# Kernel optimization log

Measured on AMD Instinct MI355X. Metric: run time of the kernel, lower is better.

## Reference

```python
import jax, jax.numpy as jnp
import numpy as np

VOCAB, EMB, HID, NCLS = 50257, 48, 128, 2000
B, S = 512, 1024


def setup_inputs() -> dict:
    key = jax.random.key(0)
    ks = jax.random.split(key, 8)
    x = jax.random.randint(ks[0], (B, S), 0, VOCAB)
    emb_table = jax.random.normal(ks[1], (VOCAB, EMB), dtype=jnp.float32)
    emb_table = emb_table.at[0].set(0.0)  # padding_idx=0
    k_ih = 1.0 / np.sqrt(HID)
    w_ih = jax.random.uniform(ks[2], (4 * HID, EMB), minval=-k_ih, maxval=k_ih, dtype=jnp.float32)
    w_hh = jax.random.uniform(ks[3], (4 * HID, HID), minval=-k_ih, maxval=k_ih, dtype=jnp.float32)
    b_ih = jax.random.uniform(ks[4], (4 * HID,), minval=-k_ih, maxval=k_ih, dtype=jnp.float32)
    b_hh = jax.random.uniform(ks[5], (4 * HID,), minval=-k_ih, maxval=k_ih, dtype=jnp.float32)
    k_fc = 1.0 / np.sqrt(HID)
    w_fc = jax.random.uniform(ks[6], (NCLS, HID), minval=-k_fc, maxval=k_fc, dtype=jnp.float32)
    b_fc = jax.random.uniform(ks[7], (NCLS,), minval=-k_fc, maxval=k_fc, dtype=jnp.float32)
    return {"x": x, "emb_table": emb_table, "w_ih": w_ih, "w_hh": w_hh,
            "b_ih": b_ih, "b_hh": b_hh, "w_fc": w_fc, "b_fc": b_fc}


def _lstm_last_hidden(e, w_ih, w_hh, b_ih, b_hh):
    # e: [B, S, E]. Precompute input contributions for all timesteps (one big GEMM).
    xg = jnp.einsum('bse,ge->bsg', e, w_ih) + b_ih + b_hh  # [B, S, 4H]
    xg = jnp.transpose(xg, (1, 0, 2))                      # [S, B, 4H]
    Bn = e.shape[0]
    h0 = jnp.zeros((Bn, HID), e.dtype)
    c0 = jnp.zeros((Bn, HID), e.dtype)

    def step(carry, xg_t):
        h, c = carry
        g = xg_t + h @ w_hh.T                              # [B, 4H]
        i, f, gg, o = jnp.split(g, 4, axis=-1)             # PyTorch gate order i,f,g,o
        i = jax.nn.sigmoid(i)
        f = jax.nn.sigmoid(f)
        gg = jnp.tanh(gg)
        o = jax.nn.sigmoid(o)
        c = f * c + i * gg
        h = o * jnp.tanh(c)
        return (h, c), None

    (h_n, _), _ = jax.lax.scan(step, (h0, c0), xg)
    return h_n


def reference(x, emb_table, w_ih, w_hh, b_ih, b_hh, w_fc, b_fc):
    e = emb_table[x]                                       # [B, S, E] gather
    h_n = _lstm_last_hidden(e, w_ih, w_hh, b_ih, b_hh)     # [B, H]
    return h_n @ w_fc.T + b_fc                             # [B, NCLS]
```

## Files before the change

### kernel.cpp

```cpp
#include <hip/hip_runtime.h>

#define DI __device__ __forceinline__

typedef unsigned int uint;
typedef unsigned short ushort;
typedef _Float16 half2t __attribute__((ext_vector_type(2)));
typedef _Float16 f16x8 __attribute__((ext_vector_type(8)));
typedef float f32x4 __attribute__((ext_vector_type(4)));

#define VOCAB 50257
#define NEMB 48
#define HID 128
#define G4 512
#define NCLS 2000
#define BATCH 512
#define SEQ 1024

DI float sigm(float x) {
  return __builtin_amdgcn_rcpf(1.0f + __builtin_amdgcn_exp2f(-1.4426950408889634f * x));
}
DI float tanhfast(float x) {
  return 1.0f - 2.0f * __builtin_amdgcn_rcpf(__builtin_amdgcn_exp2f(2.8853900817779268f * x) + 1.0f);
}

DI void barrier_lds_only() {
  asm volatile("s_waitcnt lgkmcnt(0)" ::: "memory");
  __builtin_amdgcn_s_barrier();
  asm volatile("" ::: "memory");
}

#define VROWS 32
__global__ __launch_bounds__(512) void build_P(
    const float* __restrict__ emb, const float* __restrict__ w_ih,
    const float* __restrict__ b_ih, const float* __restrict__ b_hh,
    _Float16* __restrict__ P)
{
  __shared__ __align__(16) float eL[VROWS][NEMB];
  const int tid = threadIdx.x;
  const int v0 = blockIdx.x * VROWS;
  int nrows = VOCAB - v0; if (nrows > VROWS) nrows = VROWS;

  for (int f = tid; f < nrows * NEMB; f += 512)
    eL[f / NEMB][f % NEMB] = emb[(size_t)v0 * NEMB + f];

  float w[NEMB];
  {
    const float* wr = w_ih + (size_t)tid * NEMB;
#pragma unroll
    for (int k = 0; k < NEMB; k++) w[k] = wr[k];
  }
  float bias = b_ih[tid] + b_hh[tid];
  const int pidx = ((tid & 127) << 2) + (tid >> 7);
  __syncthreads();

  for (int v = 0; v < nrows; v++) {
    const float4* e4 = (const float4*)&eL[v][0];
    float a = bias;
#pragma unroll
    for (int k = 0; k < NEMB / 4; k++) {
      float4 e = e4[k];
      a += w[4 * k] * e.x + w[4 * k + 1] * e.y + w[4 * k + 2] * e.z + w[4 * k + 3] * e.w;
    }
    P[(size_t)(v0 + v) * G4 + pidx] = (_Float16)a;
  }
}

__global__ __launch_bounds__(512, 4) void lstm_mfma5(
    const int* __restrict__ x, const float* __restrict__ w_hh,
    const _Float16* __restrict__ P, float* __restrict__ hout)
{
  __shared__ ushort tokL[SEQ];
  __shared__ __align__(16) _Float16 hbuf[2][16][HID];

  const int tid  = threadIdx.x;
  const int lane = tid & 63;
  const int wave = tid >> 6;
  const int l15  = lane & 15;
  const int lg   = lane >> 4;
  const int u    = wave * 16 + l15;
  const int blk  = blockIdx.x;

  {
    const int* xp = x + (size_t)blk * SEQ;
#pragma unroll
    for (int i = 0; i < SEQ / 512; i++) tokL[tid + 512 * i] = (ushort)xp[tid + 512 * i];
  }
  {
    uint4 z; z.x = z.y = z.z = z.w = 0u;
    ((uint4*)hbuf)[tid] = z;
  }

  f16x8 Bf[4][4];
#pragma unroll
  for (int g = 0; g < 4; g++) {
    const float* wr = w_hh + (size_t)(g * 128 + u) * HID + lg * 8;
#pragma unroll
    for (int ck = 0; ck < 4; ck++) {
      const float4* p4 = (const float4*)(wr + ck * 32);
      float4 wa = p4[0], wb = p4[1];
      f16x8 f;
      f[0] = (_Float16)wa.x; f[1] = (_Float16)wa.y;
      f[2] = (_Float16)wa.z; f[3] = (_Float16)wa.w;
      f[4] = (_Float16)wb.x; f[5] = (_Float16)wb.y;
      f[6] = (_Float16)wb.z; f[7] = (_Float16)wb.w;
      Bf[g][ck] = f;
    }
  }

  int aoff[4];
#pragma unroll
  for (int ck = 0; ck < 4; ck++)
    aoff[ck] = l15 * 256 + ((((ck * 4 + lg) ^ l15)) << 4);

  const int hwoff0 = u * 2;
  float cst0 = 0.0f;

  __syncthreads();

  uint2 xgA0 = {0, 0}, xgB0 = {0, 0};
  if (lg == 0) {
    xgA0 = *(const uint2*)(P + (size_t)tokL[0] * G4 + u * 4);
    xgB0 = *(const uint2*)(P + (size_t)tokL[1] * G4 + u * 4);
  }

  const f32x4 fz = {0.f, 0.f, 0.f, 0.f};
  const char* hB = (const char*)hbuf;
  char* hW = (char*)hbuf;

#define MF(Areg, ckk, a0, a1, a2, a3) do {                                     \
    a0 = __builtin_amdgcn_mfma_f32_16x16x32_f16(Areg, Bf[0][ckk], a0, 0, 0, 0);\
    a1 = __builtin_amdgcn_mfma_f32_16x16x32_f16(Areg, Bf[1][ckk], a1, 0, 0, 0);\
    a2 = __builtin_amdgcn_mfma_f32_16x16x32_f16(Areg, Bf[2][ckk], a2, 0, 0, 0);\
    a3 = __builtin_amdgcn_mfma_f32_16x16x32_f16(Areg, Bf[3][ckk], a3, 0, 0, 0);\
  } while (0)

#define STEP(t, par) do {                                                      \
    const char* hc = hB + (par) * 4096;                                        \
    f16x8 A0 = *(const f16x8*)(hc + aoff[0]);                                  \
    f16x8 A1 = *(const f16x8*)(hc + aoff[1]);                                  \
    f16x8 A2 = *(const f16x8*)(hc + aoff[2]);                                  \
    f16x8 A3 = *(const f16x8*)(hc + aoff[3]);                                  \
    f32x4 a0 = fz, a1 = fz, a2 = fz, a3 = fz;                                  \
    MF(A0, 0, a0, a1, a2, a3);                                                 \
    MF(A1, 1, a0, a1, a2, a3);                                                 \
    MF(A2, 2, a0, a1, a2, a3);                                                 \
    MF(A3, 3, a0, a1, a2, a3);                                                 \
    if (lg == 0) {                                                             \
      uint2 xc0 = (par) ? xgB0 : xgA0;           \
      int tc = (t) + 2; if (tc > SEQ - 1) tc = SEQ - 1;                        \
      int tk0 = tokL[tc];                                                      \
      uint2 v0 = *(const uint2*)(P + (size_t)tk0 * G4 + u * 4);                \
      if (par) xgB0 = v0; else xgA0 = v0;                                      \
      char* hn = hW + ((par) ^ 1) * 4096;                                      \
      half2t x0 = __builtin_bit_cast(half2t, xc0.x);                           \
      half2t x1 = __builtin_bit_cast(half2t, xc0.y);                           \
      float gi = a0[0] + (float)x0.x;                                          \
      float gf = a1[0] + (float)x0.y;                                          \
      float gc = a2[0] + (float)x1.x;                                          \
      float go = a3[0] + (float)x1.y;                                          \
      float fi = sigm(gi), ff = sigm(gf), gt = tanhfast(gc), fo = sigm(go);    \
      cst0 = ff * cst0 + fi * gt;                                              \
      float hh = fo * tanhfast(cst0);                                          \
      *(_Float16*)(hn + hwoff0) = (_Float16)hh;                                \
      if ((t) == SEQ - 1)                                                      \
        hout[(size_t)blk * HID + u] = hh;                                      \
    }                                                                          \
    barrier_lds_only();                                                        \
  } while (0)

  for (int t = 0; t < SEQ; t += 2) { STEP(t, 0); STEP(t + 1, 1); }
#undef STEP
#undef MF
}

typedef _Float16 h2 __attribute__((ext_vector_type(2)));
DI float fdot2f(h2 a, h2 b, float c) { return c + (float)a.x * (float)b.x + (float)a.y * (float)b.y; }

__global__ __launch_bounds__(512, 4) void lstm_scan_fb(
    const int* __restrict__ x, const float* __restrict__ emb,
    const float* __restrict__ w_ih, const float* __restrict__ w_hh,
    const float* __restrict__ b_ih, const float* __restrict__ b_hh,
    float* __restrict__ hout)
{
  __shared__ int tokL[SEQ];
  __shared__ __align__(16) _Float16 h16[HID];
  __shared__ float g2h[2][G4];
  __shared__ __align__(8) h2 e16[2][NEMB / 2];

  const int tid = threadIdx.x;
  const int b = blockIdx.x;
  const int col = tid & 255;
  const int kh = tid >> 8;
  const int koff = kh * (HID / 2);

  {
    const int* xp = x + (size_t)b * SEQ;
#pragma unroll
    for (int i = 0; i < SEQ / 512; i++) tokL[tid + 512 * i] = xp[tid + 512 * i];
  }

  h2 w0[HID / 4], w1[HID / 4];
  {
    const float4* wr0 = (const float4*)(w_hh + (size_t)col * HID + koff);
    const float4* wr1 = (const float4*)(w_hh + (size_t)(col + 256) * HID + koff);
#pragma unroll
    for (int k = 0; k < HID / 8; k++) {
      float4 a = wr0[k];
      h2 p; p.x = (_Float16)a.x; p.y = (_Float16)a.y; w0[2 * k] = p;
      p.x = (_Float16)a.z; p.y = (_Float16)a.w; w0[2 * k + 1] = p;
      float4 bv = wr1[k];
      p.x = (_Float16)bv.x; p.y = (_Float16)bv.y; w1[2 * k] = p;
      p.x = (_Float16)bv.z; p.y = (_Float16)bv.w; w1[2 * k + 1] = p;
    }
  }
  h2 wih0[NEMB / 2], wih1[NEMB / 2];
  float bias0 = 0.0f, bias1 = 0.0f;
  if (kh == 0) {
    const float* wr0 = w_ih + (size_t)col * NEMB;
    const float* wr1 = w_ih + (size_t)(col + 256) * NEMB;
#pragma unroll
    for (int k = 0; k < NEMB / 2; k++) {
      h2 p;
      p.x = (_Float16)wr0[2 * k]; p.y = (_Float16)wr0[2 * k + 1]; wih0[k] = p;
      p.x = (_Float16)wr1[2 * k]; p.y = (_Float16)wr1[2 * k + 1]; wih1[k] = p;
    }
    bias0 = b_ih[col] + b_hh[col];
    bias1 = b_ih[col + 256] + b_hh[col + 256];
  }
  if (tid < HID) h16[tid] = (_Float16)0.0f;
  __syncthreads();

  float c = 0.0f;
  float2 einfl = {0.0f, 0.0f};
  if (tid < NEMB / 2) {
    float2 e0 = ((const float2*)(emb + (size_t)tokL[0] * NEMB))[tid];
    einfl    = ((const float2*)(emb + (size_t)tokL[1] * NEMB))[tid];
    h2 p; p.x = (_Float16)e0.x; p.y = (_Float16)e0.y;
    e16[0][tid] = p;
  }
  __syncthreads();

#define STEPF(t, par) do {                                                     \
    float xg0, xg1;                                                            \
    if (tid < NEMB / 2) {                                                      \
      int tc = (t) + 2; if (tc > SEQ - 1) tc = SEQ - 1;                        \
      h2 p; p.x = (_Float16)einfl.x; p.y = (_Float16)einfl.y;                  \
      e16[((t) + 1) & 1][tid] = p;                                             \
      einfl = ((const float2*)(emb + (size_t)tokL[tc] * NEMB))[tid];           \
    }                                                                          \
    if (kh == 0) {                                                             \
      xg0 = bias0; xg1 = bias1;                                                \
      _Pragma("unroll")                                                        \
      for (int k = 0; k < NEMB / 2; k++) {                                     \
        xg0 = fdot2f(wih0[k], e16[(par)][k], xg0);                             \
        xg1 = fdot2f(wih1[k], e16[(par)][k], xg1);                             \
      }                                                                        \
    } else { xg0 = 0.0f; xg1 = 0.0f; }                                         \
    const uint4* hv = (const uint4*)h16 + (kh << 3);                           \
    float s0 = xg0, u0 = 0.0f, s1 = xg1, u1 = 0.0f;                            \
    _Pragma("unroll")                                                          \
    for (int kt = 0; kt < HID / 16; kt++) {                                    \
      uint4 hq = hv[kt];                                                       \
      h2 ha = __builtin_bit_cast(h2, hq.x);                                    \
      h2 hb = __builtin_bit_cast(h2, hq.y);                                    \
      h2 hc = __builtin_bit_cast(h2, hq.z);                                    \
      h2 hd = __builtin_bit_cast(h2, hq.w);                                    \
      s0 = fdot2f(w0[4 * kt + 0], ha, s0);                                     \
      u0 = fdot2f(w0[4 * kt + 1], hb, u0);                                     \
      s0 = fdot2f(w0[4 * kt + 2], hc, s0);                                     \
      u0 = fdot2f(w0[4 * kt + 3], hd, u0);                                     \
      s1 = fdot2f(w1[4 * kt + 0], ha, s1);                                     \
      u1 = fdot2f(w1[4 * kt + 1], hb, u1);                                     \
      s1 = fdot2f(w1[4 * kt + 2], hc, s1);                                     \
      u1 = fdot2f(w1[4 * kt + 3], hd, u1);                                     \
    }                                                                          \
    g2h[kh][col] = s0 + u0;                                                    \
    g2h[kh][col + 256] = s1 + u1;                                              \
    barrier_lds_only();                                                        \
    if (tid < HID) {                                                           \
      float gi = g2h[0][tid]           + g2h[1][tid];                          \
      float gf = g2h[0][HID + tid]     + g2h[1][HID + tid];                    \
      float gc = g2h[0][2 * HID + tid] + g2h[1][2 * HID + tid];                \
      float go = g2h[0][3 * HID + tid] + g2h[1][3 * HID + tid];                \
      float fi = sigm(gi), ff = sigm(gf), gt = tanhfast(gc), fo = sigm(go);    \
      c = ff * c + fi * gt;                                                    \
      float hh = fo * tanhfast(c);                                             \
      h16[tid] = (_Float16)hh;                                                 \
      if ((t) == SEQ - 1) hout[(size_t)b * HID + tid] = hh;                    \
    }                                                                          \
    barrier_lds_only();                                                        \
  } while (0)

  for (int t = 0; t < SEQ; t += 2) { STEPF(t, 0); STEPF(t + 1, 1); }
#undef STEPF
}

#define FCR 64
#define FCC 64
__global__ __launch_bounds__(256) void fc_kernel(
    const float* __restrict__ h, const float* __restrict__ w_fc,
    const float* __restrict__ b_fc, float* __restrict__ out)
{
  __shared__ float aT[HID][FCR];
  __shared__ float bT[HID][FCC];
  const int tid = threadIdx.x;
  const int r0 = blockIdx.y * FCR;
  const int c0 = blockIdx.x * FCC;

  for (int f = tid; f < FCR * (HID / 4); f += 256) {
    int row = f >> 5, q = f & 31;
    float4 v = ((const float4*)h)[(((size_t)(r0 + row)) << 5) + q];
    aT[4 * q + 0][row] = v.x; aT[4 * q + 1][row] = v.y;
    aT[4 * q + 2][row] = v.z; aT[4 * q + 3][row] = v.w;
    int wrow = c0 + row;
    float4 wv;
    if (wrow < NCLS) wv = ((const float4*)w_fc)[(((size_t)wrow) << 5) + q];
    else { wv.x = 0.f; wv.y = 0.f; wv.z = 0.f; wv.w = 0.f; }
    bT[4 * q + 0][row] = wv.x; bT[4 * q + 1][row] = wv.y;
    bT[4 * q + 2][row] = wv.z; bT[4 * q + 3][row] = wv.w;
  }
  __syncthreads();

  const int cr = tid & 15, rr = tid >> 4;
  float acc[4][4];
#pragma unroll
  for (int i = 0; i < 4; i++)
#pragma unroll
    for (int j = 0; j < 4; j++) acc[i][j] = 0.0f;

#pragma unroll 4
  for (int k = 0; k < HID; k++) {
    float4 av = *(const float4*)&aT[k][4 * rr];
    float4 bv = *(const float4*)&bT[k][4 * cr];
    float a[4] = {av.x, av.y, av.z, av.w};
    float bb[4] = {bv.x, bv.y, bv.z, bv.w};
#pragma unroll
    for (int i = 0; i < 4; i++)
#pragma unroll
      for (int j = 0; j < 4; j++) acc[i][j] += a[i] * bb[j];
  }

#pragma unroll
  for (int j = 0; j < 4; j++) {
    int cc = c0 + 4 * cr + j;
    if (cc < NCLS) {
      float bias = b_fc[cc];
#pragma unroll
      for (int i = 0; i < 4; i++)
        out[(size_t)(r0 + 4 * rr + i) * NCLS + cc] = acc[i][j] + bias;
    }
  }
}

extern "C" void kernel_launch(void* const* d_in, const int* in_sizes, int n_in,
                              void* d_out, int out_size, void* d_ws, size_t ws_size,
                              hipStream_t stream) {
  const int*   xx   = (const int*)d_in[0];
  const float* emb  = (const float*)d_in[1];
  const float* w_ih = (const float*)d_in[2];
  const float* w_hh = (const float*)d_in[3];
  const float* b_ih = (const float*)d_in[4];
  const float* b_hh = (const float*)d_in[5];
  const float* w_fc = (const float*)d_in[6];
  const float* b_fc = (const float*)d_in[7];
  float* out = (float*)d_out;

  const size_t pbytes = (size_t)VOCAB * G4 * sizeof(_Float16);
  const size_t palign = (pbytes + 255) & ~(size_t)255;
  const size_t hbytes = (size_t)BATCH * HID * sizeof(float);

  float* hout;
  if (ws_size >= palign + hbytes) {
    _Float16* P = (_Float16*)d_ws;
    hout = (float*)((char*)d_ws + palign);
    build_P<<<(VOCAB + VROWS - 1) / VROWS, 512, 0, stream>>>(emb, w_ih, b_ih, b_hh, P);
    lstm_mfma5<<<BATCH, 512, 0, stream>>>(xx, w_hh, P, hout);
  } else {
    hout = (float*)d_ws;
    lstm_scan_fb<<<BATCH, 512, 0, stream>>>(xx, emb, w_ih, w_hh, b_ih, b_hh, hout);
  }
  dim3 fcg((NCLS + FCC - 1) / FCC, BATCH / FCR);
  fc_kernel<<<fcg, 256, 0, stream>>>(hout, w_fc, b_fc, out);
}
```

Measured before the change: 965.4 us.

## Process two batch rows per LSTM block using spare MFMA rows

Each LSTM block now advances two sequences at once, halving the grid to 256 blocks. The second sequence occupies row 1 of the 16-row MFMA A tile, which was previously zero-padded, so the recurrent matmul per step costs about the same. Row-1 gate results are passed through a small LDS exchange buffer to lanes 16-31, which compute that sequence's cell update. The h write offset uses a swizzle that matches the A-load addressing. The intent is to get more useful work out of each latency-bound step, at the cost of an extra LDS round trip inside the step and fewer resident waves per CU.

```diff
diff --git a/kernel.cpp b/kernel.cpp
--- a/kernel.cpp
+++ b/kernel.cpp
@@ -15,6 +15,8 @@
 #define NCLS 2000
 #define BATCH 512
 #define SEQ 1024
+#define MROWS 2
+#define NBLK2 (BATCH / MROWS)
 
 DI float sigm(float x) {
   return __builtin_amdgcn_rcpf(1.0f + __builtin_amdgcn_exp2f(-1.4426950408889634f * x));
@@ -65,12 +67,13 @@
   }
 }
 
-__global__ __launch_bounds__(512, 4) void lstm_mfma5(
+__global__ __launch_bounds__(512, 2) void lstm_mfma6(
     const int* __restrict__ x, const float* __restrict__ w_hh,
     const _Float16* __restrict__ P, float* __restrict__ hout)
 {
-  __shared__ ushort tokL[SEQ];
+  __shared__ ushort tokL[MROWS][SEQ];
   __shared__ __align__(16) _Float16 hbuf[2][16][HID];
+  __shared__ float xch[8][4][16];
 
   const int tid  = threadIdx.x;
   const int lane = tid & 63;
@@ -81,9 +84,8 @@
   const int blk  = blockIdx.x;
 
   {
-    const int* xp = x + (size_t)blk * SEQ;
-#pragma unroll
-    for (int i = 0; i < SEQ / 512; i++) tokL[tid + 512 * i] = (ushort)xp[tid + 512 * i];
+    const int* xp = x + (size_t)blk * MROWS * SEQ;
+    for (int i = tid; i < MROWS * SEQ; i += 512) ((ushort*)tokL)[i] = (ushort)xp[i];
   }
   {
     uint4 z; z.x = z.y = z.z = z.w = 0u;
@@ -112,15 +114,15 @@
   for (int ck = 0; ck < 4; ck++)
     aoff[ck] = l15 * 256 + ((((ck * 4 + lg) ^ l15)) << 4);
 
-  const int hwoff0 = u * 2;
-  float cst0 = 0.0f;
-
-  __syncthreads();
-
-  uint2 xgA0 = {0, 0}, xgB0 = {0, 0};
-  if (lg == 0) {
-    xgA0 = *(const uint2*)(P + (size_t)tokL[0] * G4 + u * 4);
-    xgB0 = *(const uint2*)(P + (size_t)tokL[1] * G4 + u * 4);
+  const int hwoff = lg * 256 + (((u >> 3) ^ (lg & 1)) << 4) + (u & 7) * 2;
+  float cst = 0.0f;
+
+  __syncthreads();
+
+  uint2 xgA = {0, 0}, xgB = {0, 0};
+  if (lg < 2) {
+    xgA = *(const uint2*)(P + (size_t)tokL[lg][0] * G4 + u * 4);
+    xgB = *(const uint2*)(P + (size_t)tokL[lg][1] * G4 + u * 4);
   }
 
   const f32x4 fz = {0.f, 0.f, 0.f, 0.f};
@@ -145,25 +147,37 @@
     MF(A1, 1, a0, a1, a2, a3);                                                 \
     MF(A2, 2, a0, a1, a2, a3);                                                 \
     MF(A3, 3, a0, a1, a2, a3);                                                 \
+        \
     if (lg == 0) {                                                             \
-      uint2 xc0 = (par) ? xgB0 : xgA0;           \
+      xch[wave][0][l15] = a0[1];                                               \
+      xch[wave][1][l15] = a1[1];                                               \
+      xch[wave][2][l15] = a2[1];                                               \
+      xch[wave][3][l15] = a3[1];                                               \
+    }                                                                          \
+    if (lg < 2) {                                                              \
+      uint2 xcur = (par) ? xgB : xgA;            \
       int tc = (t) + 2; if (tc > SEQ - 1) tc = SEQ - 1;                        \
-      int tk0 = tokL[tc];                                                      \
-      uint2 v0 = *(const uint2*)(P + (size_t)tk0 * G4 + u * 4);                \
-      if (par) xgB0 = v0; else xgA0 = v0;                                      \
-      char* hn = hW + ((par) ^ 1) * 4096;                                      \
-      half2t x0 = __builtin_bit_cast(half2t, xc0.x);                           \
-      half2t x1 = __builtin_bit_cast(half2t, xc0.y);                           \
-      float gi = a0[0] + (float)x0.x;                                          \
-      float gf = a1[0] + (float)x0.y;                                          \
-      float gc = a2[0] + (float)x1.x;                                          \
-      float go = a3[0] + (float)x1.y;                                          \
+      int tk = tokL[lg][tc];                                                   \
+      uint2 v = *(const uint2*)(P + (size_t)tk * G4 + u * 4);                  \
+      if (par) xgB = v; else xgA = v;                                          \
+      float v0, v1, v2, v3;                                                    \
+      if (lg == 0) { v0 = a0[0]; v1 = a1[0]; v2 = a2[0]; v3 = a3[0]; }         \
+      else {                                                                   \
+        v0 = xch[wave][0][l15]; v1 = xch[wave][1][l15];                        \
+        v2 = xch[wave][2][l15]; v3 = xch[wave][3][l15];                        \
+      }                                                                        \
+      half2t x0 = __builtin_bit_cast(half2t, xcur.x);                          \
+      half2t x1 = __builtin_bit_cast(half2t, xcur.y);                          \
+      float gi = v0 + (float)x0.x;                                             \
+      float gf = v1 + (float)x0.y;                                             \
+      float gc = v2 + (float)x1.x;                                             \
+      float go = v3 + (float)x1.y;                                             \
       float fi = sigm(gi), ff = sigm(gf), gt = tanhfast(gc), fo = sigm(go);    \
-      cst0 = ff * cst0 + fi * gt;                                              \
-      float hh = fo * tanhfast(cst0);                                          \
-      *(_Float16*)(hn + hwoff0) = (_Float16)hh;                                \
+      cst = ff * cst + fi * gt;                                                \
+      float hh = fo * tanhfast(cst);                                           \
+      *(_Float16*)(hW + ((par) ^ 1) * 4096 + hwoff) = (_Float16)hh;            \
       if ((t) == SEQ - 1)                                                      \
-        hout[(size_t)blk * HID + u] = hh;                                      \
+        hout[((size_t)blk * MROWS + lg) * HID + u] = hh;                       \
     }                                                                          \
     barrier_lds_only();                                                        \
   } while (0)
@@ -374,7 +388,7 @@
     _Float16* P = (_Float16*)d_ws;
     hout = (float*)((char*)d_ws + palign);
     build_P<<<(VOCAB + VROWS - 1) / VROWS, 512, 0, stream>>>(emb, w_ih, b_ih, b_hh, P);
-    lstm_mfma5<<<BATCH, 512, 0, stream>>>(xx, w_hh, P, hout);
+    lstm_mfma6<<<NBLK2, 512, 0, stream>>>(xx, w_hh, P, hout);
   } else {
     hout = (float*)d_ws;
     lstm_scan_fb<<<BATCH, 512, 0, stream>>>(xx, emb, w_ih, w_hh, b_ih, b_hh, hout);
```

After: 826.6 us. 1.17x faster.
